# Performance work log

Measured on AMD Instinct MI355X. Metric: run time of the kernel, lower is better.

Reference implementation:

```python
import jax, jax.numpy as jnp
import numpy as np

D_MODEL, D_STATE, D_CONV, EXPAND = 1024, 16, 4, 2
D_INNER = EXPAND * D_MODEL            # 2048
DT_RANK = -(-D_MODEL // 16)           # ceil(d_model/16) = 64


def setup_inputs() -> dict:
    key = jax.random.key(0)
    ks = jax.random.split(key, 9)
    B, L = 2, 2048
    x = jax.random.normal(ks[0], (B, L, D_MODEL), dtype=jnp.float32)
    s = 0.02
    W_in = jax.random.normal(ks[1], (2 * D_INNER, D_MODEL), dtype=jnp.float32) * s
    conv_w = jax.random.normal(ks[2], (D_INNER, 1, D_CONV), dtype=jnp.float32) * 0.1
    conv_b = jax.random.normal(ks[3], (D_INNER,), dtype=jnp.float32) * 0.01
    W_xproj = jax.random.normal(ks[4], (DT_RANK + 2 * D_STATE, D_INNER), dtype=jnp.float32) * s
    W_dt = jax.random.normal(ks[5], (D_INNER, DT_RANK), dtype=jnp.float32) * (DT_RANK ** -0.5)
    b_dt = jnp.log(jnp.exp(jax.random.uniform(ks[6], (D_INNER,), minval=1e-3, maxval=0.1)) - 1.0)  # inv-softplus init
    A_log = jnp.log(jnp.broadcast_to(jnp.arange(1, D_STATE + 1, dtype=jnp.float32), (D_INNER, D_STATE)))
    Dskip = jnp.ones((D_INNER,), dtype=jnp.float32)
    W_out = jax.random.normal(ks[7], (D_MODEL, D_INNER), dtype=jnp.float32) * s
    return {"x": x, "W_in": W_in, "conv_w": conv_w, "conv_b": conv_b,
            "W_xproj": W_xproj, "W_dt": W_dt, "b_dt": b_dt,
            "A_log": A_log, "Dskip": Dskip, "W_out": W_out}


def _mamba_fwd(x, W_in, conv_w, conv_b, W_xproj, W_dt, b_dt, A_log, Dskip, W_out):
    Bsz, L, _ = x.shape
    # in_proj -> split into x branch and gate z
    xz = jnp.einsum('bld,ed->ble', x, W_in)               # (B,L,2*d_inner)
    xb, z = jnp.split(xz, 2, axis=-1)
    # causal depthwise conv1d over time
    xc = jnp.transpose(xb, (0, 2, 1))                      # (B,d_inner,L)
    xc = jax.lax.conv_general_dilated(
        xc, conv_w, window_strides=(1,), padding=[(D_CONV - 1, 0)],
        dimension_numbers=('NCH', 'OIH', 'NCH'), feature_group_count=D_INNER)
    u = jax.nn.silu(jnp.transpose(xc, (0, 2, 1)) + conv_b)  # (B,L,d_inner)
    # input-dependent SSM params
    x_dbl = jnp.einsum('bld,ed->ble', u, W_xproj)          # (B,L,dt_rank+2n)
    dt_low, Bmat, Cmat = jnp.split(x_dbl, [DT_RANK, DT_RANK + D_STATE], axis=-1)
    delta = jax.nn.softplus(jnp.einsum('blr,dr->bld', dt_low, W_dt) + b_dt)  # (B,L,d_inner)
    A = -jnp.exp(A_log)                                    # (d_inner,d_state)

    def step(h, inp):
        dt_t, u_t, B_t, C_t = inp                          # (B,d),(B,d),(B,n),(B,n)
        dA = jnp.exp(dt_t[:, :, None] * A)                 # (B,d,n)
        h = dA * h + (dt_t * u_t)[:, :, None] * B_t[:, None, :]
        y_t = jnp.einsum('bdn,bn->bd', h, C_t)
        return h, y_t

    h0 = jnp.zeros((Bsz, D_INNER, D_STATE), dtype=x.dtype)
    xs = (jnp.transpose(delta, (1, 0, 2)), jnp.transpose(u, (1, 0, 2)),
          jnp.transpose(Bmat, (1, 0, 2)), jnp.transpose(Cmat, (1, 0, 2)))
    _, ys = jax.lax.scan(step, h0, xs)                     # (L,B,d_inner)
    y = jnp.transpose(ys, (1, 0, 2)) + u * Dskip           # skip connection
    y = y * jax.nn.silu(z)                                 # gating
    return jnp.einsum('bld,ed->ble', y, W_out)             # (B,L,d_model)


def reference(x, W_in, conv_w, conv_b, W_xproj, W_dt, b_dt, A_log, Dskip, W_out):
    return _mamba_fwd(x, W_in, conv_w, conv_b, W_xproj, W_dt, b_dt, A_log, Dskip, W_out)
```

## Files before the change

kernel.cpp:

```cpp
#include <hip/hip_runtime.h>
#include <math.h>

#define MB_B      2
#define MB_L      2048
#define MB_DMODEL 1024
#define MB_DINNER 2048
#define MB_DSTATE 16
#define MB_DTRANK 64
#define MB_ROWS   (MB_B * MB_L)
#define MB_E2     (2 * MB_DINNER)
#define SC_NC     16
#define SC_CHUNK  (MB_L / SC_NC)
#define SC_CL     32
#define SC_CB     64
#define CV_R      8

typedef _Float16 f16;
typedef __attribute__((ext_vector_type(4))) _Float16 half4;
typedef __attribute__((ext_vector_type(8))) _Float16 half8;
typedef __attribute__((ext_vector_type(4))) float floatx4;

__device__ __forceinline__ float softplus_f(float x) {
    return (x > 20.f) ? x : log1pf(expf(x));
}
__device__ __forceinline__ float silu_f(float x) {
    return x / (1.f + expf(-x));
}

#if __has_builtin(__builtin_amdgcn_exp2f)
__device__ __forceinline__ float exp2_fast(float x) {
    return __builtin_amdgcn_exp2f(x);
}
#else
__device__ __forceinline__ float exp2_fast(float x) {
    return __expf(0.69314718056f * x);
}
#endif

typedef const __attribute__((address_space(1))) unsigned char gbyte;
typedef __attribute__((address_space(3))) unsigned char lbyte;
__device__ __forceinline__ void gl_lds16(const void* g, void* l) {
    __builtin_amdgcn_global_load_lds((gbyte*)g, (lbyte*)l, 16, 0, 0);
}

template <int CTRL>
__device__ __forceinline__ float dpp_add(float x) {
    int xi = __builtin_bit_cast(int, x);
    int yi = __builtin_amdgcn_update_dpp(0, xi, CTRL, 0xF, 0xF, true);
    return x + __builtin_bit_cast(float, yi);
}

__global__ __launch_bounds__(256) void convert_all_kernel(
    const float* __restrict__ x, const float* __restrict__ W_in,
    const float* __restrict__ W_xproj, const float* __restrict__ W_dt,
    const float* __restrict__ W_out, f16* __restrict__ dst)
{
    const int i = (blockIdx.x * 256 + threadIdx.x) * 8;
    const float* src;
    int local, nsrc;
    if (i < 4194304)      { src = x;       local = i;           nsrc = 4194304; }
    else if (i < 8388608) { src = W_in;    local = i - 4194304; nsrc = 4194304; }
    else if (i < 8650752) { src = W_xproj; local = i - 8388608; nsrc = 196608; }
    else if (i < 8781824) { src = W_dt;    local = i - 8650752; nsrc = 131072; }
    else                  { src = W_out;   local = i - 8781824; nsrc = 2097152; }
    half8 o;
    if (local < nsrc) {
        const float4 a = *reinterpret_cast<const float4*>(src + local);
        const float4 b = *reinterpret_cast<const float4*>(src + local + 4);
        o[0] = (f16)a.x; o[1] = (f16)a.y; o[2] = (f16)a.z; o[3] = (f16)a.w;
        o[4] = (f16)b.x; o[5] = (f16)b.y; o[6] = (f16)b.z; o[7] = (f16)b.w;
    } else {
#pragma unroll
        for (int j = 0; j < 8; j++) o[j] = (f16)0.f;
    }
    *reinterpret_cast<half8*>(dst + i) = o;
}

template <typename OutT, int EPI, int BM, int GN>
__global__ __launch_bounds__(256) void gemm_mfma(
    const f16* __restrict__ A, int lda,
    const f16* __restrict__ B, int ldb,
    OutT* __restrict__ C, int ldc, int K,
    const float* __restrict__ bias)
{
    constexpr int BN = 128;
    constexpr int GM = 4 / GN;
    constexpr int WM = BM / GM;
    constexpr int WN = BN / GN;
    constexpr int MT = WM / 16, NT = WN / 16;
    constexpr int CPW = (BM + BN) / 32;

    __shared__ f16 As[BM * 64];
    __shared__ f16 Bs[BN * 64];

    const int tid  = threadIdx.x;
    const int lane = tid & 63;
    const int wave = tid >> 6;
    const int wr   = wave / GN, wc = wave % GN;
    const int bm   = blockIdx.y * BM, bn = blockIdx.x * BN;

    floatx4 zero4 = {0.f, 0.f, 0.f, 0.f};
    floatx4 acc[MT][NT];
#pragma unroll
    for (int i = 0; i < MT; i++)
#pragma unroll
        for (int j = 0; j < NT; j++) acc[i][j] = zero4;

    const int srow = lane >> 3;
    const int scol = ((lane & 7) ^ (srow & 7)) * 8;
    const f16* gp[CPW];
    f16* lp[CPW];
#pragma unroll
    for (int i = 0; i < CPW; i++) {
        const int rbase = (wave * CPW + i) * 8;
        if (rbase < BM) {
            gp[i] = A + (size_t)(bm + rbase + srow) * lda + scol;
            lp[i] = As + rbase * 64;
        } else {
            gp[i] = B + (size_t)(bn + (rbase - BM) + srow) * ldb + scol;
            lp[i] = Bs + (rbase - BM) * 64;
        }
    }

    const int mr = lane & 15;
    const int ko = lane >> 4;

    for (int k0 = 0; k0 < K; k0 += 64) {
#pragma unroll
        for (int i = 0; i < CPW; i++) gl_lds16(gp[i] + k0, lp[i]);
        __syncthreads();

        half8 af[MT][2], bf[NT][2];
#pragma unroll
        for (int kk = 0; kk < 2; kk++) {
            const int koff = ((ko + kk * 4) ^ (mr & 7)) * 8;
#pragma unroll
            for (int mt = 0; mt < MT; mt++)
                af[mt][kk] = *reinterpret_cast<const half8*>(
                    As + (wr * WM + mt * 16 + mr) * 64 + koff);
#pragma unroll
            for (int nt = 0; nt < NT; nt++)
                bf[nt][kk] = *reinterpret_cast<const half8*>(
                    Bs + (wc * WN + nt * 16 + mr) * 64 + koff);
        }
#pragma unroll
        for (int kk = 0; kk < 2; kk++)
#pragma unroll
            for (int mt = 0; mt < MT; mt++)
#pragma unroll
                for (int nt = 0; nt < NT; nt++)
                    acc[mt][nt] = __builtin_amdgcn_mfma_f32_16x16x32_f16(
                        af[mt][kk], bf[nt][kk], acc[mt][nt], 0, 0, 0);
        __syncthreads();
    }

    const int rbase = (lane >> 4) * 4;
#pragma unroll
    for (int mt = 0; mt < MT; mt++) {
        const int row0 = bm + wr * WM + mt * 16 + rbase;
#pragma unroll
        for (int nt = 0; nt < NT; nt++) {
            const int col = bn + wc * WN + nt * 16 + mr;
#pragma unroll
            for (int r = 0; r < 4; r++) {
                float v = acc[mt][nt][r];
                if constexpr (EPI == 1) v = softplus_f(v + bias[col]);
                C[(size_t)(row0 + r) * ldc + col] = (OutT)v;
            }
        }
    }
}

__global__ __launch_bounds__(256) void gemm3_splitk(
    const f16* __restrict__ A, const f16* __restrict__ B,
    float* __restrict__ Cp)
{
    __shared__ f16 As[128 * 32];
    __shared__ f16 Bs[128 * 32];

    const int tid  = threadIdx.x;
    const int lane = tid & 63;
    const int wave = tid >> 6;
    const int wr   = wave >> 1, wc = wave & 1;
    const int bm   = blockIdx.y * 128;
    const int kbeg = blockIdx.x * 256;

    floatx4 zero4 = {0.f, 0.f, 0.f, 0.f};
    floatx4 acc[4][4];
#pragma unroll
    for (int i = 0; i < 4; i++)
#pragma unroll
        for (int j = 0; j < 4; j++) acc[i][j] = zero4;

    const int srow = lane >> 2;
    const int scol = ((lane & 3) ^ ((srow >> 1) & 3)) * 8;
    const f16* gA0 = A + (size_t)(bm + wave * 32 + srow) * MB_DINNER + scol;
    const f16* gA1 = A + (size_t)(bm + wave * 32 + 16 + srow) * MB_DINNER + scol;
    const f16* gB0 = B + (size_t)(wave * 32 + srow) * MB_DINNER + scol;
    const f16* gB1 = B + (size_t)(wave * 32 + 16 + srow) * MB_DINNER + scol;
    f16* lA0 = As + wave * 1024;
    f16* lA1 = As + wave * 1024 + 512;
    f16* lB0 = Bs + wave * 1024;
    f16* lB1 = Bs + wave * 1024 + 512;

    const int mr = lane & 15;
    const int kq = ((lane >> 4) ^ ((mr >> 1) & 3)) * 8;

    for (int k0 = kbeg; k0 < kbeg + 256; k0 += 32) {
        gl_lds16(gA0 + k0, lA0);
        gl_lds16(gA1 + k0, lA1);
        gl_lds16(gB0 + k0, lB0);
        gl_lds16(gB1 + k0, lB1);
        __syncthreads();

        half8 af[4], bf[4];
#pragma unroll
        for (int mt = 0; mt < 4; mt++)
            af[mt] = *reinterpret_cast<const half8*>(
                As + (wr * 64 + mt * 16 + mr) * 32 + kq);
#pragma unroll
        for (int nt = 0; nt < 4; nt++)
            bf[nt] = *reinterpret_cast<const half8*>(
                Bs + (wc * 64 + nt * 16 + mr) * 32 + kq);
#pragma unroll
        for (int mt = 0; mt < 4; mt++)
#pragma unroll
            for (int nt = 0; nt < 4; nt++)
                acc[mt][nt] = __builtin_amdgcn_mfma_f32_16x16x32_f16(
                    af[mt], bf[nt], acc[mt][nt], 0, 0, 0);
        __syncthreads();
    }

    float* Co = Cp + (size_t)blockIdx.x * MB_ROWS * 128;
    const int rbase = (lane >> 4) * 4;
#pragma unroll
    for (int mt = 0; mt < 4; mt++) {
        const int row0 = bm + wr * 64 + mt * 16 + rbase;
#pragma unroll
        for (int nt = 0; nt < 4; nt++) {
            const int col = wc * 64 + nt * 16 + mr;
#pragma unroll
            for (int r = 0; r < 4; r++)
                Co[(size_t)(row0 + r) * 128 + col] = acc[mt][nt][r];
        }
    }
}

__global__ __launch_bounds__(256) void reduce_xdbl_kernel(
    const float* __restrict__ Cp, float* __restrict__ xdbl,
    f16* __restrict__ xdbl_h)
{
    const int t = blockIdx.x * 256 + threadIdx.x;
    const int row = t >> 5, c4 = (t & 31) * 4;
    float4 s = {0.f, 0.f, 0.f, 0.f};
#pragma unroll
    for (int j = 0; j < 8; j++) {
        const float4 v = *reinterpret_cast<const float4*>(
            Cp + (size_t)j * MB_ROWS * 128 + (size_t)row * 128 + c4);
        s.x += v.x; s.y += v.y; s.z += v.z; s.w += v.w;
    }
    if (c4 < 96)
        *reinterpret_cast<float4*>(xdbl + (size_t)row * 96 + c4) = s;
    half4 h = {(f16)s.x, (f16)s.y, (f16)s.z, (f16)s.w};
    *reinterpret_cast<half4*>(xdbl_h + (size_t)row * 128 + c4) = h;
}

__global__ __launch_bounds__(256) void conv_silu_kernel(
    const f16* __restrict__ xz, const float* __restrict__ cw,
    const float* __restrict__ cb, f16* __restrict__ u)
{
    const int tid  = threadIdx.x;
    const int dv   = tid * 8;
    const int rbeg = blockIdx.x * CV_R;
    const int l0   = rbeg & (MB_L - 1);

    float wt[8][4];
#pragma unroll
    for (int j = 0; j < 8; j++) {
        const float4 wv = *reinterpret_cast<const float4*>(cw + (dv + j) * 4);
        wt[j][0] = wv.x; wt[j][1] = wv.y; wt[j][2] = wv.z; wt[j][3] = wv.w;
    }
    float bias[8];
    {
        const float4 b0 = *reinterpret_cast<const float4*>(cb + dv);
        const float4 b1 = *reinterpret_cast<const float4*>(cb + dv + 4);
        bias[0] = b0.x; bias[1] = b0.y; bias[2] = b0.z; bias[3] = b0.w;
        bias[4] = b1.x; bias[5] = b1.y; bias[6] = b1.z; bias[7] = b1.w;
    }

    half8 xr[CV_R + 3];
#pragma unroll
    for (int i = 0; i < 3; i++) {
        if (l0 >= 3 - i) {
            xr[i] = *reinterpret_cast<const half8*>(
                xz + (size_t)(rbeg - 3 + i) * MB_E2 + dv);
        } else {
#pragma unroll
            for (int j = 0; j < 8; j++) xr[i][j] = (f16)0.f;
        }
    }
#pragma unroll
    for (int r = 0; r < CV_R; r++)
        xr[3 + r] = *reinterpret_cast<const half8*>(
            xz + (size_t)(rbeg + r) * MB_E2 + dv);

#pragma unroll
    for (int r = 0; r < CV_R; r++) {
        float acc[8];
#pragma unroll
        for (int j = 0; j < 8; j++) acc[j] = bias[j];
#pragma unroll
        for (int k = 0; k < 4; k++) {
            const half8 xv = xr[r + k];
#pragma unroll
            for (int j = 0; j < 8; j++)
                acc[j] = fmaf((float)xv[j], wt[j][k], acc[j]);
        }
        half8 o;
#pragma unroll
        for (int j = 0; j < 8; j++) o[j] = (f16)silu_f(acc[j]);
        *reinterpret_cast<half8*>(u + (size_t)(rbeg + r) * MB_DINNER + dv) = o;
    }
}

__global__ __launch_bounds__(256) void scan_pass1(
    const f16*  __restrict__ delta,
    const f16*  __restrict__ u,
    const float* __restrict__ xdbl,
    const float* __restrict__ A_log,
    float* __restrict__ Hc,
    float* __restrict__ Pc)
{
    __shared__ float2 sDU[SC_CB][SC_CL + 1];
    __shared__ float  sB[SC_CL][20];

    const int tid   = threadIdx.x;
    const int lane  = tid & 63;
    const int wave  = tid >> 6;
    const int cg    = (lane >> 2) & 15;
    const int q     = lane & 3;
    const int ch    = wave * 16 + cg;
    const int cb    = blockIdx.x & 63;
    const int chunk = blockIdx.x >> 6;
    const int gchan = cb * SC_CB + ch;
    const int b     = gchan >> 11;
    const int dbase = (cb & 31) * SC_CB;
    const int d     = dbase + ch;
    const int lbeg  = chunk * SC_CHUNK;

    const size_t base2048 = (size_t)b * MB_L * MB_DINNER;
    const size_t base96   = (size_t)b * MB_L * 96;

    const float4 alog = *reinterpret_cast<const float4*>(
        A_log + d * MB_DSTATE + q * 4);
    float Av2[4] = {-expf(alog.x) * 1.44269504f, -expf(alog.y) * 1.44269504f,
                    -expf(alog.z) * 1.44269504f, -expf(alog.w) * 1.44269504f};
    float h[4] = {0.f, 0.f, 0.f, 0.f};
    float sdt = 0.f;

    const int lloc  = tid >> 3;
    const int c8    = (tid & 7) * 8;
    const int cpair = (tid & 7) * 2;

    half8 pD, pU; float2 pB;
    auto stage_load = [&](int l0) {
        const size_t row = (size_t)(l0 + lloc);
        pD = *reinterpret_cast<const half8*>(
            delta + base2048 + row * MB_DINNER + dbase + c8);
        pU = *reinterpret_cast<const half8*>(
            u + base2048 + row * MB_DINNER + dbase + c8);
        pB = *reinterpret_cast<const float2*>(
            xdbl + base96 + row * 96 + MB_DTRANK + cpair);
    };
    auto stage_write = [&]() {
#pragma unroll
        for (int j = 0; j < 8; j++) {
            const float dd = (float)pD[j], uu = (float)pU[j];
            sDU[c8 + j][lloc] = make_float2(dd, dd * uu);
        }
        *reinterpret_cast<float2*>(&sB[lloc][cpair]) = pB;
    };

    stage_load(lbeg);
    stage_write();
    __syncthreads();

    for (int l0 = lbeg; l0 < lbeg + SC_CHUNK; l0 += SC_CL) {
        const bool has_next = (l0 + SC_CL) < lbeg + SC_CHUNK;
        if (has_next) stage_load(l0 + SC_CL);

#pragma unroll
        for (int ll = 0; ll < SC_CL; ll++) {
            const float2 du = sDU[ch][ll];
            const float4 Bv = *reinterpret_cast<const float4*>(&sB[ll][q * 4]);
            h[0] = fmaf(exp2_fast(du.x * Av2[0]), h[0], du.y * Bv.x);
            h[1] = fmaf(exp2_fast(du.x * Av2[1]), h[1], du.y * Bv.y);
            h[2] = fmaf(exp2_fast(du.x * Av2[2]), h[2], du.y * Bv.z);
            h[3] = fmaf(exp2_fast(du.x * Av2[3]), h[3], du.y * Bv.w);
            sdt += du.x;
        }
        __syncthreads();
        if (has_next) stage_write();
        __syncthreads();
    }

    const size_t cidx = ((size_t)chunk * MB_ROWS + gchan) * MB_DSTATE + q * 4;
    float4 H4 = {h[0], h[1], h[2], h[3]};
    float4 P4 = {exp2_fast(Av2[0] * sdt), exp2_fast(Av2[1] * sdt),
                 exp2_fast(Av2[2] * sdt), exp2_fast(Av2[3] * sdt)};
    *reinterpret_cast<float4*>(Hc + cidx) = H4;
    *reinterpret_cast<float4*>(Pc + cidx) = P4;
}

__global__ __launch_bounds__(256) void scan_pass2(
    const f16*  __restrict__ delta,
    const f16*  __restrict__ u,
    const float* __restrict__ xdbl,
    const float* __restrict__ A_log,
    const float* __restrict__ Dskip,
    const f16*  __restrict__ xz,
    const float* __restrict__ Hc,
    const float* __restrict__ Pc,
    f16* __restrict__ yg)
{
    __shared__ float2 sDU[SC_CB][SC_CL + 1];
    __shared__ float2 sGS[SC_CB][SC_CL + 1];
    __shared__ float  sB[SC_CL][20];
    __shared__ float  sC[SC_CL][20];

    const int tid   = threadIdx.x;
    const int lane  = tid & 63;
    const int wave  = tid >> 6;
    const int cg    = (lane >> 2) & 15;
    const int q     = lane & 3;
    const int ch    = wave * 16 + cg;
    const int cb    = blockIdx.x & 63;
    const int chunk = blockIdx.x >> 6;
    const int gchan = cb * SC_CB + ch;
    const int b     = gchan >> 11;
    const int dbase = (cb & 31) * SC_CB;
    const int d     = dbase + ch;
    const int lbeg  = chunk * SC_CHUNK;

    const size_t base2048 = (size_t)b * MB_L * MB_DINNER;
    const size_t base4096 = (size_t)b * MB_L * MB_E2;
    const size_t base96   = (size_t)b * MB_L * 96;

    const float4 alog = *reinterpret_cast<const float4*>(
        A_log + d * MB_DSTATE + q * 4);
    float Av2[4] = {-expf(alog.x) * 1.44269504f, -expf(alog.y) * 1.44269504f,
                    -expf(alog.z) * 1.44269504f, -expf(alog.w) * 1.44269504f};

    const int lloc  = tid >> 3;
    const int c8    = (tid & 7) * 8;
    const int cpair = (tid & 7) * 2;

    float Dsk8[8];
    {
        const float4 d0 = *reinterpret_cast<const float4*>(Dskip + dbase + c8);
        const float4 d1 = *reinterpret_cast<const float4*>(Dskip + dbase + c8 + 4);
        Dsk8[0] = d0.x; Dsk8[1] = d0.y; Dsk8[2] = d0.z; Dsk8[3] = d0.w;
        Dsk8[4] = d1.x; Dsk8[5] = d1.y; Dsk8[6] = d1.z; Dsk8[7] = d1.w;
    }

    half8 pD, pU, pZ; float2 pB, pC;
    auto stage_load = [&](int l0) {
        const size_t row = (size_t)(l0 + lloc);
        pD = *reinterpret_cast<const half8*>(
            delta + base2048 + row * MB_DINNER + dbase + c8);
        pU = *reinterpret_cast<const half8*>(
            u + base2048 + row * MB_DINNER + dbase + c8);
        pZ = *reinterpret_cast<const half8*>(
            xz + base4096 + row * MB_E2 + MB_DINNER + dbase + c8);
        pB = *reinterpret_cast<const float2*>(
            xdbl + base96 + row * 96 + MB_DTRANK + cpair);
        pC = *reinterpret_cast<const float2*>(
            xdbl + base96 + row * 96 + MB_DTRANK + MB_DSTATE + cpair);
    };
    auto stage_write = [&]() {
#pragma unroll
        for (int j = 0; j < 8; j++) {
            const float dd = (float)pD[j], uu = (float)pU[j];
            sDU[c8 + j][lloc] = make_float2(dd, dd * uu);
            const float g = silu_f((float)pZ[j]);
            sGS[c8 + j][lloc] = make_float2(g, uu * Dsk8[j] * g);
        }
        *reinterpret_cast<float2*>(&sB[lloc][cpair]) = pB;
        *reinterpret_cast<float2*>(&sC[lloc][cpair]) = pC;
    };

    stage_load(lbeg);

    float h[4] = {0.f, 0.f, 0.f, 0.f};
    for (int j = 0; j < chunk; j++) {
        const size_t cidx = ((size_t)j * MB_ROWS + gchan) * MB_DSTATE + q * 4;
        const float4 P4 = *reinterpret_cast<const float4*>(Pc + cidx);
        const float4 H4 = *reinterpret_cast<const float4*>(Hc + cidx);
        h[0] = fmaf(P4.x, h[0], H4.x);
        h[1] = fmaf(P4.y, h[1], H4.y);
        h[2] = fmaf(P4.z, h[2], H4.z);
        h[3] = fmaf(P4.w, h[3], H4.w);
    }

    stage_write();
    __syncthreads();

    for (int l0 = lbeg; l0 < lbeg + SC_CHUNK; l0 += SC_CL) {
        const bool has_next = (l0 + SC_CL) < lbeg + SC_CHUNK;
        if (has_next) stage_load(l0 + SC_CL);

        float y[SC_CL / 4] = {0.f, 0.f, 0.f, 0.f, 0.f, 0.f, 0.f, 0.f};
#pragma unroll
        for (int ll = 0; ll < SC_CL; ll++) {
            const float2 du = sDU[ch][ll];
            const float4 Bv = *reinterpret_cast<const float4*>(&sB[ll][q * 4]);
            const float4 Cv = *reinterpret_cast<const float4*>(&sC[ll][q * 4]);
            h[0] = fmaf(exp2_fast(du.x * Av2[0]), h[0], du.y * Bv.x);
            h[1] = fmaf(exp2_fast(du.x * Av2[1]), h[1], du.y * Bv.y);
            h[2] = fmaf(exp2_fast(du.x * Av2[2]), h[2], du.y * Bv.z);
            h[3] = fmaf(exp2_fast(du.x * Av2[3]), h[3], du.y * Bv.w);
            float p = h[0] * Cv.x;
            p = fmaf(h[1], Cv.y, p);
            p = fmaf(h[2], Cv.z, p);
            p = fmaf(h[3], Cv.w, p);
            p = dpp_add<0xB1>(p);
            p = dpp_add<0x4E>(p);
            y[ll >> 2] = (q == (ll & 3)) ? p : y[ll >> 2];
        }

#pragma unroll
        for (int k = 0; k < SC_CL / 4; k++) {
            const float2 gs = sGS[ch][4 * k + q];
            yg[base2048 + (size_t)(l0 + 4 * k + q) * MB_DINNER + dbase + ch] =
                (f16)fmaf(y[k], gs.x, gs.y);
        }

        __syncthreads();
        if (has_next) stage_write();
        __syncthreads();
    }
}

extern "C" void kernel_launch(void* const* d_in, const int* in_sizes, int n_in,
                              void* d_out, int out_size, void* d_ws,
                              size_t ws_size, hipStream_t stream)
{
    const float* x      = (const float*)d_in[0];
    const float* W_in   = (const float*)d_in[1];
    const float* conv_w = (const float*)d_in[2];
    const float* conv_b = (const float*)d_in[3];
    const float* W_xproj= (const float*)d_in[4];
    const float* W_dt   = (const float*)d_in[5];
    const float* b_dt   = (const float*)d_in[6];
    const float* A_log  = (const float*)d_in[7];
    const float* Dskip  = (const float*)d_in[8];
    const float* W_out  = (const float*)d_in[9];
    float* out = (float*)d_out;

    char* p = (char*)d_ws;
    f16* xz_h    = (f16*)p;  p += (size_t)MB_ROWS * MB_E2 * 2;
    f16* u_h     = (f16*)p;  p += (size_t)MB_ROWS * MB_DINNER * 2;
    f16* delta_h = (f16*)p;  p += (size_t)MB_ROWS * MB_DINNER * 2;
    f16* yg_h    = (f16*)p;  p += (size_t)MB_ROWS * MB_DINNER * 2;
    float* xdbl  = (float*)p; p += (size_t)MB_ROWS * 96 * 4;
    f16* xdbl_h  = (f16*)p;  p += (size_t)MB_ROWS * 128 * 2;
    f16* x_h     = (f16*)p;  p += (size_t)MB_ROWS * MB_DMODEL * 2;
    f16* W_inh   = (f16*)p;  p += (size_t)MB_E2 * MB_DMODEL * 2;
    f16* W_xprojh= (f16*)p;  p += (size_t)128 * MB_DINNER * 2;
    f16* W_dth   = (f16*)p;  p += (size_t)MB_DINNER * MB_DTRANK * 2;
    f16* W_outh  = (f16*)p;  p += (size_t)MB_DMODEL * MB_DINNER * 2;
    float* Hc    = (float*)p; p += (size_t)SC_NC * MB_ROWS * MB_DSTATE * 4;
    float* Pc    = (float*)p; p += (size_t)SC_NC * MB_ROWS * MB_DSTATE * 4;
    float* Cp    = (float*)p;

    const dim3 blk(256);

    convert_all_kernel<<<5312, blk, 0, stream>>>(
        x, W_in, W_xproj, W_dt, W_out, x_h);

    gemm_mfma<f16, 0, 128, 2><<<dim3(32, 32), blk, 0, stream>>>(
        x_h, MB_DMODEL, W_inh, MB_DMODEL, xz_h, MB_E2, MB_DMODEL, nullptr);

    conv_silu_kernel<<<MB_ROWS / CV_R, blk, 0, stream>>>(
        xz_h, conv_w, conv_b, u_h);

    gemm3_splitk<<<dim3(8, 32), blk, 0, stream>>>(u_h, W_xprojh, Cp);
    reduce_xdbl_kernel<<<512, blk, 0, stream>>>(Cp, xdbl, xdbl_h);

    gemm_mfma<f16, 1, 128, 2><<<dim3(16, 32), blk, 0, stream>>>(
        xdbl_h, 128, W_dth, MB_DTRANK, delta_h, MB_DINNER, MB_DTRANK, b_dt);

    scan_pass1<<<(SC_NC - 1) * 64, blk, 0, stream>>>(
        delta_h, u_h, xdbl, A_log, Hc, Pc);

    scan_pass2<<<SC_NC * 64, blk, 0, stream>>>(
        delta_h, u_h, xdbl, A_log, Dskip, xz_h, Hc, Pc, yg_h);

    gemm_mfma<float, 0, 64, 4><<<dim3(8, 64), blk, 0, stream>>>(
        yg_h, MB_DINNER, W_outh, MB_DINNER, out, MB_DMODEL, MB_DINNER, nullptr);
}
```

Baseline: 314.6 us.

## Store scan shared-memory staging in half precision and double scan chunk count

Result: no change. 308.7 us (-1.9%).

```diff
diff --git a/kernel.cpp b/kernel.cpp
--- a/kernel.cpp
+++ b/kernel.cpp
@@ -9,13 +9,14 @@
 #define MB_DTRANK 64
 #define MB_ROWS   (MB_B * MB_L)
 #define MB_E2     (2 * MB_DINNER)
-#define SC_NC     16
+#define SC_NC     32
 #define SC_CHUNK  (MB_L / SC_NC)
 #define SC_CL     32
 #define SC_CB     64
-#define CV_R      8
+#define CV_R      4
 
 typedef _Float16 f16;
+typedef __attribute__((ext_vector_type(2))) _Float16 half2v;
 typedef __attribute__((ext_vector_type(4))) _Float16 half4;
 typedef __attribute__((ext_vector_type(8))) _Float16 half8;
 typedef __attribute__((ext_vector_type(4))) float floatx4;
@@ -331,7 +332,7 @@
     float* __restrict__ Hc,
     float* __restrict__ Pc)
 {
-    __shared__ float2 sDU[SC_CB][SC_CL + 1];
+    __shared__ half2v sDU[SC_CB][SC_CL + 2];
     __shared__ float  sB[SC_CL][20];
 
     const int tid   = threadIdx.x;
@@ -375,8 +376,8 @@
     auto stage_write = [&]() {
 #pragma unroll
         for (int j = 0; j < 8; j++) {
-            const float dd = (float)pD[j], uu = (float)pU[j];
-            sDU[c8 + j][lloc] = make_float2(dd, dd * uu);
+            half2v t; t[0] = pD[j]; t[1] = pD[j] * pU[j];
+            sDU[c8 + j][lloc] = t;
         }
         *reinterpret_cast<float2*>(&sB[lloc][cpair]) = pB;
     };
@@ -391,13 +392,14 @@
 
 #pragma unroll
         for (int ll = 0; ll < SC_CL; ll++) {
-            const float2 du = sDU[ch][ll];
+            const half2v duh = sDU[ch][ll];
+            const float dx = (float)duh[0], dy = (float)duh[1];
             const float4 Bv = *reinterpret_cast<const float4*>(&sB[ll][q * 4]);
-            h[0] = fmaf(exp2_fast(du.x * Av2[0]), h[0], du.y * Bv.x);
-            h[1] = fmaf(exp2_fast(du.x * Av2[1]), h[1], du.y * Bv.y);
-            h[2] = fmaf(exp2_fast(du.x * Av2[2]), h[2], du.y * Bv.z);
-            h[3] = fmaf(exp2_fast(du.x * Av2[3]), h[3], du.y * Bv.w);
-            sdt += du.x;
+            h[0] = fmaf(exp2_fast(dx * Av2[0]), h[0], dy * Bv.x);
+            h[1] = fmaf(exp2_fast(dx * Av2[1]), h[1], dy * Bv.y);
+            h[2] = fmaf(exp2_fast(dx * Av2[2]), h[2], dy * Bv.z);
+            h[3] = fmaf(exp2_fast(dx * Av2[3]), h[3], dy * Bv.w);
+            sdt += dx;
         }
         __syncthreads();
         if (has_next) stage_write();
@@ -423,8 +425,8 @@
     const float* __restrict__ Pc,
     f16* __restrict__ yg)
 {
-    __shared__ float2 sDU[SC_CB][SC_CL + 1];
-    __shared__ float2 sGS[SC_CB][SC_CL + 1];
+    __shared__ half2v sDU[SC_CB][SC_CL + 2];
+    __shared__ half2v sGS[SC_CB][SC_CL + 2];
     __shared__ float  sB[SC_CL][20];
     __shared__ float  sC[SC_CL][20];
 
@@ -480,10 +482,12 @@
     auto stage_write = [&]() {
 #pragma unroll
         for (int j = 0; j < 8; j++) {
-            const float dd = (float)pD[j], uu = (float)pU[j];
-            sDU[c8 + j][lloc] = make_float2(dd, dd * uu);
+            half2v t; t[0] = pD[j]; t[1] = pD[j] * pU[j];
+            sDU[c8 + j][lloc] = t;
+            const float uu = (float)pU[j];
             const float g = silu_f((float)pZ[j]);
-            sGS[c8 + j][lloc] = make_float2(g, uu * Dsk8[j] * g);
+            half2v gs; gs[0] = (f16)g; gs[1] = (f16)(uu * Dsk8[j] * g);
+            sGS[c8 + j][lloc] = gs;
         }
         *reinterpret_cast<float2*>(&sB[lloc][cpair]) = pB;
         *reinterpret_cast<float2*>(&sC[lloc][cpair]) = pC;
@@ -512,13 +516,14 @@
         float y[SC_CL / 4] = {0.f, 0.f, 0.f, 0.f, 0.f, 0.f, 0.f, 0.f};
 #pragma unroll
         for (int ll = 0; ll < SC_CL; ll++) {
-            const float2 du = sDU[ch][ll];
+            const half2v duh = sDU[ch][ll];
+            const float dx = (float)duh[0], dy = (float)duh[1];
             const float4 Bv = *reinterpret_cast<const float4*>(&sB[ll][q * 4]);
             const float4 Cv = *reinterpret_cast<const float4*>(&sC[ll][q * 4]);
-            h[0] = fmaf(exp2_fast(du.x * Av2[0]), h[0], du.y * Bv.x);
-            h[1] = fmaf(exp2_fast(du.x * Av2[1]), h[1], du.y * Bv.y);
-            h[2] = fmaf(exp2_fast(du.x * Av2[2]), h[2], du.y * Bv.z);
-            h[3] = fmaf(exp2_fast(du.x * Av2[3]), h[3], du.y * Bv.w);
+            h[0] = fmaf(exp2_fast(dx * Av2[0]), h[0], dy * Bv.x);
+            h[1] = fmaf(exp2_fast(dx * Av2[1]), h[1], dy * Bv.y);
+            h[2] = fmaf(exp2_fast(dx * Av2[2]), h[2], dy * Bv.z);
+            h[3] = fmaf(exp2_fast(dx * Av2[3]), h[3], dy * Bv.w);
             float p = h[0] * Cv.x;
             p = fmaf(h[1], Cv.y, p);
             p = fmaf(h[2], Cv.z, p);
@@ -530,9 +535,9 @@
 
 #pragma unroll
         for (int k = 0; k < SC_CL / 4; k++) {
-            const float2 gs = sGS[ch][4 * k + q];
+            const half2v gs = sGS[ch][4 * k + q];
             yg[base2048 + (size_t)(l0 + 4 * k + q) * MB_DINNER + dbase + ch] =
-                (f16)fmaf(y[k], gs.x, gs.y);
+                (f16)fmaf(y[k], (float)gs[0], (float)gs[1]);
         }
 
         __syncthreads();
@@ -569,9 +574,9 @@
     f16* W_xprojh= (f16*)p;  p += (size_t)128 * MB_DINNER * 2;
     f16* W_dth   = (f16*)p;  p += (size_t)MB_DINNER * MB_DTRANK * 2;
     f16* W_outh  = (f16*)p;  p += (size_t)MB_DMODEL * MB_DINNER * 2;
-    float* Hc    = (float*)p; p += (size_t)SC_NC * MB_ROWS * MB_DSTATE * 4;
-    float* Pc    = (float*)p; p += (size_t)SC_NC * MB_ROWS * MB_DSTATE * 4;
     float* Cp    = (float*)p;
+    float* Hc    = Cp;
+    float* Pc    = Cp + (size_t)SC_NC * MB_ROWS * MB_DSTATE;
 
     const dim3 blk(256);
 
```
